# Kernel tuning notes

Measured on AMD Instinct MI355X. Metric: run time of the kernel, lower is better.

The kernel has to match this reference:

```python
import jax, jax.numpy as jnp
import numpy as np

WINDOW = 7
SHIFT = 3
HEADS = 4


def _rel_pos_index(w):
    # same construction as ShiftedWindowAttention.__init__ (numpy, static)
    coords = np.stack(np.meshgrid(np.arange(w), np.arange(w), indexing='ij'))  # [2,w,w]
    cf = coords.reshape(2, -1)                       # [2, w*w]
    rc = (cf[:, :, None] - cf[:, None, :]).transpose(1, 2, 0)  # [L,L,2]
    rc[:, :, 0] += w - 1
    rc[:, :, 1] += w - 1
    rc[:, :, 0] *= 2 * w - 1
    return rc.sum(-1).reshape(-1)                    # [L*L]


def _attn_mask(H, W, w, s):
    # cyclic-shift attention mask, static numpy constant
    m = np.zeros((H, W))
    slices = ((0, -w), (-w, -s), (-s, None))
    cnt = 0
    for hs in slices:
        for ws in slices:
            m[hs[0]:hs[1], ws[0]:ws[1]] = cnt
            cnt += 1
    m = m.reshape(H // w, w, W // w, w).transpose(0, 2, 1, 3).reshape(-1, w * w)  # [nwin, L]
    d = m[:, None, :] - m[:, :, None]                # [nwin, L, L]
    return np.where(d != 0, -100.0, 0.0).astype(np.float32)


def setup_inputs() -> dict:
    key = jax.random.key(0)
    ks = jax.random.split(key, 6)
    B, H, W, C = 64, 56, 56, 128
    return {
        'x': jax.random.normal(ks[0], (B, H, W, C), dtype=jnp.float32),
        'qkv_weight': jax.random.normal(ks[1], (3 * C, C), dtype=jnp.float32) * 0.02,
        'qkv_bias': jax.random.normal(ks[2], (3 * C,), dtype=jnp.float32) * 0.02,
        'proj_weight': jax.random.normal(ks[3], (C, C), dtype=jnp.float32) * 0.02,
        'proj_bias': jax.random.normal(ks[4], (C,), dtype=jnp.float32) * 0.02,
        'rel_bias_table': jax.random.normal(ks[5], ((2 * WINDOW - 1) ** 2, HEADS), dtype=jnp.float32) * 0.02,
    }


def reference(x, qkv_weight, qkv_bias, proj_weight, proj_bias, rel_bias_table):
    B, H, W, C = x.shape
    w, s, h = WINDOW, SHIFT, HEADS
    d = C // h
    nH, nW = H // w, W // w
    nwin = nH * nW
    L = w * w

    # relative position bias: [h, L, L]
    bias = rel_bias_table[jnp.asarray(_rel_pos_index(w))].reshape(L, L, h).transpose(2, 0, 1)

    # cyclic shift + window partition -> [B*nwin, L, C]
    xs = jnp.roll(x, (-s, -s), axis=(1, 2))
    xw = xs.reshape(B, nH, w, nW, w, C).transpose(0, 1, 3, 2, 4, 5).reshape(B * nwin, L, C)

    # fused qkv projection (F.linear: x @ W.T + b)
    qkv = (xw @ qkv_weight.T + qkv_bias).reshape(B * nwin, L, 3, h, d).transpose(2, 0, 3, 1, 4)
    q, k, v = qkv[0] * (d ** -0.5), qkv[1], qkv[2]   # each [B*nwin, h, L, d]

    attn = jnp.einsum('nhqd,nhkd->nhqk', q, k) + bias[None]
    mask = jnp.asarray(_attn_mask(H, W, w, s))       # [nwin, L, L]
    attn = attn.reshape(B, nwin, h, L, L) + mask[None, :, None]
    attn = jax.nn.softmax(attn.reshape(B * nwin, h, L, L), axis=-1)

    out = jnp.einsum('nhqk,nhkd->nhqd', attn, v).transpose(0, 2, 1, 3).reshape(B * nwin, L, C)
    out = out @ proj_weight.T + proj_bias

    # window merge + reverse shift -> [B, H, W, C]
    out = out.reshape(B, nH, nW, w, w, C).transpose(0, 1, 3, 2, 4, 5).reshape(B, H, W, C)
    return jnp.roll(out, (s, s), axis=(1, 2))
```

## Files before the change

kernel.cpp:

```cpp
#include <hip/hip_runtime.h>

typedef __attribute__((ext_vector_type(8))) short short8;
typedef __attribute__((ext_vector_type(4))) float f32x4;

static __device__ __forceinline__ unsigned short f2bf(float f) {
  union { float f; unsigned int u; } v; v.f = f;
  unsigned int r = v.u + 0x7FFFu + ((v.u >> 16) & 1u);
  return (unsigned short)(r >> 16);
}
static __device__ __forceinline__ unsigned int pack2(float a, float b) {
  return (unsigned int)f2bf(a) | ((unsigned int)f2bf(b) << 16);
}

#define KO 0
#define VO 2560
#define PO 4864
#define WSTRIDE 7424

__global__ __launch_bounds__(256) void k_prep(const float* __restrict__ wq,
    const float* __restrict__ wp, const float* __restrict__ tbl,
    unsigned short* __restrict__ dq, unsigned short* __restrict__ dp,
    unsigned short* __restrict__ biasH) {
  const int n = blockIdx.x * 256 + threadIdx.x;
  if (n < 384 * 128) dq[n] = f2bf(wq[n]);
  if (n < 128 * 128) dp[n] = f2bf(wp[n]);
  if (n < 65536) {
    const int j = n & 63, i = (n >> 6) & 63;
    const int h = (n >> 12) & 3, bb = (n >> 14) & 1, aa = (n >> 15) & 1;
    float val;
    if (i >= 49) val = 0.0f;
    else if (j >= 49) val = -1e30f;
    else {
      const int ih = i / 7, iw = i - ih * 7, jh = j / 7, jw = j - jh * 7;
      const int didx = (ih - jh + 6) * 13 + (iw - jw + 6);
      const int irg = (aa ? (ih < 4 ? 3 : 6) : 0) + (bb ? (iw < 4 ? 1 : 2) : 0);
      const int jrg = (aa ? (jh < 4 ? 3 : 6) : 0) + (bb ? (jw < 4 ? 1 : 2) : 0);
      val = tbl[didx * 4 + h] - (irg != jrg ? 100.0f : 0.0f);
    }
    biasH[n] = f2bf(val);
  }
}

__global__ __launch_bounds__(256) void k_prepx(const float* __restrict__ x,
    unsigned short* __restrict__ xw) {
  const int idx = blockIdx.x * 256 + threadIdx.x;
  const int row = idx >> 4;
  const int c8 = idx & 15;
  const int win = row / 49;
  const int t = row - win * 49;
  const int b = win >> 6, wl = win & 63;
  const int wh = wl >> 3, ww = wl & 7;
  const int th = t / 7, tw = t - th * 7;
  int sh = wh * 7 + th + 3; if (sh >= 56) sh -= 56;
  int sw = ww * 7 + tw + 3; if (sw >= 56) sw -= 56;
  const float4* src = (const float4*)(x + (((size_t)(b * 56 + sh)) * 56 + sw) * 128 + c8 * 8);
  float4 fa = src[0], fb = src[1];
  uint4 u;
  u.x = pack2(fa.x, fa.y); u.y = pack2(fa.z, fa.w);
  u.z = pack2(fb.x, fb.y); u.w = pack2(fb.z, fb.w);
  *(uint4*)(xw + (size_t)row * 128 + c8 * 8) = u;
}

__global__ __launch_bounds__(256, 2) void k_fused(const unsigned short* __restrict__ xw,
    const unsigned short* __restrict__ Wq, const float* __restrict__ qb,
    const unsigned short* __restrict__ Wp, const float* __restrict__ pb,
    const unsigned short* __restrict__ biasH, float* __restrict__ out) {
  __shared__ __align__(16) unsigned short lds[4 * WSTRIDE];
  const int tid = threadIdx.x;
  const int win = blockIdx.x;
  const int b = win >> 6, wl = win & 63;
  const int wh = wl >> 3, ww = wl & 7;
  const int wv = tid >> 6, ln = tid & 63;
  const int l15 = ln & 15, l4 = ln >> 4;
  unsigned short* W = lds + wv * WSTRIDE;

  const unsigned short* bmB = biasH
      + ((((wh == 7 ? 2 : 0) + (ww == 7 ? 1 : 0)) * 4 + wv) << 12)
      + l15 * 64 + 4 * l4;
  uint2 bm16[4][4];
#pragma unroll
  for (int mt = 0; mt < 4; ++mt)
#pragma unroll
    for (int nt = 0; nt < 4; ++nt)
      bm16[mt][nt] = *(const uint2*)(bmB + mt * 1024 + nt * 16);

  const unsigned short* rp[4];
  bool vld[4];
#pragma unroll
  for (int mt = 0; mt < 4; ++mt) {
    const int t = mt * 16 + l15;
    vld[mt] = (t < 49);
    rp[mt] = xw + ((size_t)win * 49 + (vld[mt] ? t : 0)) * 128;
  }
  int nrow[6];
#pragma unroll
  for (int j = 0; j < 6; ++j)
    nrow[j] = (j >> 1) * 128 + wv * 32 + (j & 1) * 16 + l15;

  const f32x4 z4 = {0.f, 0.f, 0.f, 0.f};
  f32x4 aS[4][4], aV[4][2];
#pragma unroll
  for (int mt = 0; mt < 4; ++mt) {
#pragma unroll
    for (int j = 0; j < 4; ++j) aS[mt][j] = z4;
#pragma unroll
    for (int j = 0; j < 2; ++j) aV[mt][j] = z4;
  }
#pragma unroll
  for (int ks = 0; ks < 4; ++ks) {
    short8 af[4], bf[6];
#pragma unroll
    for (int mt = 0; mt < 4; ++mt) {
      uint4 u = *(const uint4*)(rp[mt] + ks * 32 + l4 * 8);
      u.x = vld[mt] ? u.x : 0u; u.y = vld[mt] ? u.y : 0u;
      u.z = vld[mt] ? u.z : 0u; u.w = vld[mt] ? u.w : 0u;
      af[mt] = *(short8*)&u;
    }
#pragma unroll
    for (int j = 0; j < 6; ++j)
      bf[j] = *(const short8*)&Wq[(size_t)nrow[j] * 128 + ks * 32 + l4 * 8];
#pragma unroll
    for (int mt = 0; mt < 4; ++mt) {
#pragma unroll
      for (int j = 0; j < 4; ++j)
        aS[mt][j] = __builtin_amdgcn_mfma_f32_16x16x32_bf16(bf[j], af[mt], aS[mt][j], 0, 0, 0);
#pragma unroll
      for (int j = 0; j < 2; ++j)
        aV[mt][j] = __builtin_amdgcn_mfma_f32_16x16x32_bf16(af[mt], bf[4 + j], aV[mt][j], 0, 0, 0);
    }
  }
  {
    const float SC = 0.17677669529663687f;
    const float4 bq0 = *(const float4*)(qb + wv * 32 + 4 * l4);
    const float4 bq1 = *(const float4*)(qb + wv * 32 + 16 + 4 * l4);
    const float4 bk0 = *(const float4*)(qb + 128 + wv * 32 + 4 * l4);
    const float4 bk1 = *(const float4*)(qb + 128 + wv * 32 + 16 + 4 * l4);
    const float bv0 = qb[256 + wv * 32 + l15];
    const float bv1 = qb[256 + wv * 32 + 16 + l15];
#pragma unroll
    for (int mt = 0; mt < 4; ++mt) {
      const int t = mt * 16 + l15;
      uint2 u;
      u.x = pack2((aS[mt][0][0] + bq0.x) * SC, (aS[mt][0][1] + bq0.y) * SC);
      u.y = pack2((aS[mt][0][2] + bq0.z) * SC, (aS[mt][0][3] + bq0.w) * SC);
      *(uint2*)&W[PO + t * 40 + 4 * l4] = u;
      u.x = pack2((aS[mt][1][0] + bq1.x) * SC, (aS[mt][1][1] + bq1.y) * SC);
      u.y = pack2((aS[mt][1][2] + bq1.z) * SC, (aS[mt][1][3] + bq1.w) * SC);
      *(uint2*)&W[PO + t * 40 + 16 + 4 * l4] = u;
      u.x = pack2(aS[mt][2][0] + bk0.x, aS[mt][2][1] + bk0.y);
      u.y = pack2(aS[mt][2][2] + bk0.z, aS[mt][2][3] + bk0.w);
      *(uint2*)&W[KO + t * 40 + 4 * l4] = u;
      u.x = pack2(aS[mt][3][0] + bk1.x, aS[mt][3][1] + bk1.y);
      u.y = pack2(aS[mt][3][2] + bk1.z, aS[mt][3][3] + bk1.w);
      *(uint2*)&W[KO + t * 40 + 16 + 4 * l4] = u;
      u.x = pack2(aV[mt][0][0] + bv0, aV[mt][0][1] + bv0);
      u.y = pack2(aV[mt][0][2] + bv0, aV[mt][0][3] + bv0);
      *(uint2*)&W[VO + l15 * 72 + mt * 16 + 4 * l4] = u;
      u.x = pack2(aV[mt][1][0] + bv1, aV[mt][1][1] + bv1);
      u.y = pack2(aV[mt][1][2] + bv1, aV[mt][1][3] + bv1);
      *(uint2*)&W[VO + (16 + l15) * 72 + mt * 16 + 4 * l4] = u;
    }
  }

  f32x4 s[4][4];
#pragma unroll
  for (int mt = 0; mt < 4; ++mt)
#pragma unroll
    for (int nt = 0; nt < 4; ++nt) s[mt][nt] = z4;
  {
    short8 qf[4], kf[4];
#pragma unroll
    for (int mt = 0; mt < 4; ++mt)
      qf[mt] = *(const short8*)&W[PO + (mt * 16 + l15) * 40 + l4 * 8];
#pragma unroll
    for (int nt = 0; nt < 4; ++nt)
      kf[nt] = *(const short8*)&W[KO + (nt * 16 + l15) * 40 + l4 * 8];
#pragma unroll
    for (int mt = 0; mt < 4; ++mt)
#pragma unroll
      for (int nt = 0; nt < 4; ++nt)
        s[mt][nt] = __builtin_amdgcn_mfma_f32_16x16x32_bf16(kf[nt], qf[mt], s[mt][nt], 0, 0, 0);
  }

  float pmax[4] = {-1e30f, -1e30f, -1e30f, -1e30f};
#pragma unroll
  for (int mt = 0; mt < 4; ++mt) {
#pragma unroll
    for (int nt = 0; nt < 4; ++nt) {
      const uint2 u = bm16[mt][nt];
      s[mt][nt][0] += __uint_as_float(u.x << 16);
      s[mt][nt][1] += __uint_as_float(u.x & 0xFFFF0000u);
      s[mt][nt][2] += __uint_as_float(u.y << 16);
      s[mt][nt][3] += __uint_as_float(u.y & 0xFFFF0000u);
      pmax[mt] = fmaxf(pmax[mt], fmaxf(fmaxf(s[mt][nt][0], s[mt][nt][1]),
                                       fmaxf(s[mt][nt][2], s[mt][nt][3])));
    }
  }
  float inv[4];
#pragma unroll
  for (int mt = 0; mt < 4; ++mt) {
    float m0 = pmax[mt];
    m0 = fmaxf(m0, __shfl_xor(m0, 16));
    m0 = fmaxf(m0, __shfl_xor(m0, 32));
    float sum = 0.0f;
#pragma unroll
    for (int nt = 0; nt < 4; ++nt)
#pragma unroll
      for (int r = 0; r < 4; ++r) {
        const float v = s[mt][nt][r];
        const float e = (v > -1e29f) ? __expf(v - m0) : 0.0f;
        s[mt][nt][r] = e;
        sum += e;
      }
    sum += __shfl_xor(sum, 16);
    sum += __shfl_xor(sum, 32);
    inv[mt] = 1.0f / sum;
  }

  f32x4 o[4][2];
#pragma unroll
  for (int mt = 0; mt < 4; ++mt)
#pragma unroll
    for (int dt = 0; dt < 2; ++dt) o[mt][dt] = z4;
#pragma unroll
  for (int mt = 0; mt < 4; ++mt) {
    const int i = mt * 16 + l15;
    if (i < 49) {
#pragma unroll
      for (int nt = 0; nt < 2; ++nt) {
        uint2 u;
        u.x = pack2(s[mt][nt][0] * inv[mt], s[mt][nt][1] * inv[mt]);
        u.y = pack2(s[mt][nt][2] * inv[mt], s[mt][nt][3] * inv[mt]);
        *(uint2*)&W[PO + i * 40 + nt * 16 + 4 * l4] = u;
      }
    }
  }
  {
    short8 pa[4], vb[2];
#pragma unroll
    for (int mt = 0; mt < 4; ++mt)
      pa[mt] = *(const short8*)&W[PO + (mt * 16 + l15) * 40 + l4 * 8];
#pragma unroll
    for (int dt = 0; dt < 2; ++dt)
      vb[dt] = *(const short8*)&W[VO + (dt * 16 + l15) * 72 + l4 * 8];
#pragma unroll
    for (int mt = 0; mt < 4; ++mt)
#pragma unroll
      for (int dt = 0; dt < 2; ++dt)
        o[mt][dt] = __builtin_amdgcn_mfma_f32_16x16x32_bf16(vb[dt], pa[mt], o[mt][dt], 0, 0, 0);
  }
#pragma unroll
  for (int mt = 0; mt < 4; ++mt) {
    const int i = mt * 16 + l15;
    if (i < 49) {
#pragma unroll
      for (int nt = 2; nt < 4; ++nt) {
        uint2 u;
        u.x = pack2(s[mt][nt][0] * inv[mt], s[mt][nt][1] * inv[mt]);
        u.y = pack2(s[mt][nt][2] * inv[mt], s[mt][nt][3] * inv[mt]);
        *(uint2*)&W[PO + i * 40 + (nt - 2) * 16 + 4 * l4] = u;
      }
    }
  }
  {
    short8 pa[4], vb[2];
#pragma unroll
    for (int mt = 0; mt < 4; ++mt)
      pa[mt] = *(const short8*)&W[PO + (mt * 16 + l15) * 40 + l4 * 8];
#pragma unroll
    for (int dt = 0; dt < 2; ++dt)
      vb[dt] = *(const short8*)&W[VO + (dt * 16 + l15) * 72 + 32 + l4 * 8];
#pragma unroll
    for (int mt = 0; mt < 4; ++mt)
#pragma unroll
      for (int dt = 0; dt < 2; ++dt)
        o[mt][dt] = __builtin_amdgcn_mfma_f32_16x16x32_bf16(vb[dt], pa[mt], o[mt][dt], 0, 0, 0);
  }
#pragma unroll
  for (int mt = 0; mt < 4; ++mt) {
    const int t = mt * 16 + l15;
#pragma unroll
    for (int dt = 0; dt < 2; ++dt) {
      uint2 u;
      u.x = pack2(o[mt][dt][0], o[mt][dt][1]);
      u.y = pack2(o[mt][dt][2], o[mt][dt][3]);
      *(uint2*)&W[KO + t * 40 + dt * 16 + 4 * l4] = u;
    }
  }
  __syncthreads();

  const float4 pbv0 = *(const float4*)(pb + wv * 32 + 4 * l4);
  const float4 pbv1 = *(const float4*)(pb + wv * 32 + 16 + 4 * l4);
  f32x4 c2[4][2];
#pragma unroll
  for (int mt = 0; mt < 4; ++mt)
#pragma unroll
    for (int nt = 0; nt < 2; ++nt) c2[mt][nt] = z4;
#pragma unroll
  for (int ks = 0; ks < 4; ++ks) {
    short8 a2[4], bp[2];
#pragma unroll
    for (int mt = 0; mt < 4; ++mt)
      a2[mt] = *(const short8*)&lds[ks * WSTRIDE + KO + (mt * 16 + l15) * 40 + l4 * 8];
#pragma unroll
    for (int nt = 0; nt < 2; ++nt)
      bp[nt] = *(const short8*)&Wp[(size_t)(wv * 32 + nt * 16 + l15) * 128 + ks * 32 + l4 * 8];
#pragma unroll
    for (int mt = 0; mt < 4; ++mt)
#pragma unroll
      for (int nt = 0; nt < 2; ++nt)
        c2[mt][nt] = __builtin_amdgcn_mfma_f32_16x16x32_bf16(bp[nt], a2[mt], c2[mt][nt], 0, 0, 0);
  }
#pragma unroll
  for (int mt = 0; mt < 4; ++mt) {
    const int t = mt * 16 + l15;
    if (t < 49) {
      const int th = t / 7, tw = t - th * 7;
      int y = wh * 7 + th + 3; if (y >= 56) y -= 56;
      int xx = ww * 7 + tw + 3; if (xx >= 56) xx -= 56;
      float* dstp = out + (((size_t)(b * 56 + y)) * 56 + xx) * 128 + wv * 32 + 4 * l4;
      float4 v0, v1;
      v0.x = c2[mt][0][0] + pbv0.x; v0.y = c2[mt][0][1] + pbv0.y;
      v0.z = c2[mt][0][2] + pbv0.z; v0.w = c2[mt][0][3] + pbv0.w;
      *(float4*)(dstp) = v0;
      v1.x = c2[mt][1][0] + pbv1.x; v1.y = c2[mt][1][1] + pbv1.y;
      v1.z = c2[mt][1][2] + pbv1.z; v1.w = c2[mt][1][3] + pbv1.w;
      *(float4*)(dstp + 16) = v1;
    }
  }
}

extern "C" void kernel_launch(void* const* d_in, const int* in_sizes, int n_in,
                              void* d_out, int out_size, void* d_ws, size_t ws_size,
                              hipStream_t stream) {
  const float* x     = (const float*)d_in[0];
  const float* qkvw  = (const float*)d_in[1];
  const float* qkvb  = (const float*)d_in[2];
  const float* projw = (const float*)d_in[3];
  const float* projb = (const float*)d_in[4];
  const float* table = (const float*)d_in[5];
  float* out = (float*)d_out;
  char* ws = (char*)d_ws;
  unsigned short* xw    = (unsigned short*)ws;
  unsigned short* Wq    = (unsigned short*)(ws + 51380224);
  unsigned short* Wp    = (unsigned short*)(ws + 51478528);
  unsigned short* biasH = (unsigned short*)(ws + 51511296);

  k_prep<<<dim3(256), dim3(256), 0, stream>>>(qkvw, projw, table, Wq, Wp, biasH);
  k_prepx<<<dim3(12544), dim3(256), 0, stream>>>(x, xw);
  k_fused<<<dim3(4096), dim3(256), 0, stream>>>(xw, Wq, qkvb, Wp, projb, biasH, out);
}
```

Measured before the change: 167.5 us.

## Split each window's query rows across two blocks to raise parallelism and cut registers

Each window is now handled by two blocks, and each block computes half of the query rows, 32 of the 64 padded tokens. K and V are still computed in full by both blocks. The V projection is moved into its own second pass, and the shared-memory layout is shrunk, to lower register pressure and LDS use, and the min-blocks launch bound is dropped. The intent is higher occupancy and more blocks in flight. The cost is that the K/V projections are computed twice per window, and the xw/Wq reads are repeated.

Measured after the change: 560.2 us. +234.4%, slower.

```diff
diff --git a/kernel.cpp b/kernel.cpp
--- a/kernel.cpp
+++ b/kernel.cpp
@@ -12,10 +12,10 @@
   return (unsigned int)f2bf(a) | ((unsigned int)f2bf(b) << 16);
 }
 
-#define KO 0
-#define VO 2560
-#define PO 4864
-#define WSTRIDE 7424
+#define QP 0
+#define KB 1280
+#define VB 3840
+#define WSTR 6144
 
 __global__ __launch_bounds__(256) void k_prep(const float* __restrict__ wq,
     const float* __restrict__ wp, const float* __restrict__ tbl,
@@ -61,25 +61,26 @@
   *(uint4*)(xw + (size_t)row * 128 + c8 * 8) = u;
 }
 
-__global__ __launch_bounds__(256, 2) void k_fused(const unsigned short* __restrict__ xw,
+__global__ __launch_bounds__(256) void k_fused(const unsigned short* __restrict__ xw,
     const unsigned short* __restrict__ Wq, const float* __restrict__ qb,
     const unsigned short* __restrict__ Wp, const float* __restrict__ pb,
     const unsigned short* __restrict__ biasH, float* __restrict__ out) {
-  __shared__ __align__(16) unsigned short lds[4 * WSTRIDE];
+  __shared__ __align__(16) unsigned short lds[4 * WSTR];
   const int tid = threadIdx.x;
-  const int win = blockIdx.x;
+  const int bid = blockIdx.x;
+  const int win = bid >> 1, half = bid & 1;
   const int b = win >> 6, wl = win & 63;
   const int wh = wl >> 3, ww = wl & 7;
   const int wv = tid >> 6, ln = tid & 63;
   const int l15 = ln & 15, l4 = ln >> 4;
-  unsigned short* W = lds + wv * WSTRIDE;
+  unsigned short* W = lds + wv * WSTR;
 
   const unsigned short* bmB = biasH
       + ((((wh == 7 ? 2 : 0) + (ww == 7 ? 1 : 0)) * 4 + wv) << 12)
-      + l15 * 64 + 4 * l4;
-  uint2 bm16[4][4];
-#pragma unroll
-  for (int mt = 0; mt < 4; ++mt)
+      + half * 2048 + l15 * 64 + 4 * l4;
+  uint2 bm16[2][4];
+#pragma unroll
+  for (int mt = 0; mt < 2; ++mt)
 #pragma unroll
     for (int nt = 0; nt < 4; ++nt)
       bm16[mt][nt] = *(const uint2*)(bmB + mt * 1024 + nt * 16);
@@ -92,23 +93,20 @@
     vld[mt] = (t < 49);
     rp[mt] = xw + ((size_t)win * 49 + (vld[mt] ? t : 0)) * 128;
   }
-  int nrow[6];
-#pragma unroll
-  for (int j = 0; j < 6; ++j)
-    nrow[j] = (j >> 1) * 128 + wv * 32 + (j & 1) * 16 + l15;
-
   const f32x4 z4 = {0.f, 0.f, 0.f, 0.f};
-  f32x4 aS[4][4], aV[4][2];
-#pragma unroll
-  for (int mt = 0; mt < 4; ++mt) {
-#pragma unroll
-    for (int j = 0; j < 4; ++j) aS[mt][j] = z4;
-#pragma unroll
-    for (int j = 0; j < 2; ++j) aV[mt][j] = z4;
-  }
+
+  f32x4 aQ[2][2], aK[4][2];
+#pragma unroll
+  for (int mt = 0; mt < 2; ++mt)
+#pragma unroll
+    for (int dt = 0; dt < 2; ++dt) aQ[mt][dt] = z4;
+#pragma unroll
+  for (int nt = 0; nt < 4; ++nt)
+#pragma unroll
+    for (int dt = 0; dt < 2; ++dt) aK[nt][dt] = z4;
 #pragma unroll
   for (int ks = 0; ks < 4; ++ks) {
-    short8 af[4], bf[6];
+    short8 af[4], bfq[2], bfk[2];
 #pragma unroll
     for (int mt = 0; mt < 4; ++mt) {
       uint4 u = *(const uint4*)(rp[mt] + ks * 32 + l4 * 8);
@@ -117,17 +115,20 @@
       af[mt] = *(short8*)&u;
     }
 #pragma unroll
-    for (int j = 0; j < 6; ++j)
-      bf[j] = *(const short8*)&Wq[(size_t)nrow[j] * 128 + ks * 32 + l4 * 8];
-#pragma unroll
-    for (int mt = 0; mt < 4; ++mt) {
-#pragma unroll
-      for (int j = 0; j < 4; ++j)
-        aS[mt][j] = __builtin_amdgcn_mfma_f32_16x16x32_bf16(bf[j], af[mt], aS[mt][j], 0, 0, 0);
-#pragma unroll
-      for (int j = 0; j < 2; ++j)
-        aV[mt][j] = __builtin_amdgcn_mfma_f32_16x16x32_bf16(af[mt], bf[4 + j], aV[mt][j], 0, 0, 0);
-    }
+    for (int dt = 0; dt < 2; ++dt) {
+      bfq[dt] = *(const short8*)&Wq[(size_t)(wv * 32 + dt * 16 + l15) * 128 + ks * 32 + l4 * 8];
+      bfk[dt] = *(const short8*)&Wq[(size_t)(128 + wv * 32 + dt * 16 + l15) * 128 + ks * 32 + l4 * 8];
+    }
+#pragma unroll
+    for (int mt = 0; mt < 2; ++mt)
+#pragma unroll
+      for (int dt = 0; dt < 2; ++dt)
+        aQ[mt][dt] = __builtin_amdgcn_mfma_f32_16x16x32_bf16(bfq[dt], af[half * 2 + mt], aQ[mt][dt], 0, 0, 0);
+#pragma unroll
+    for (int nt = 0; nt < 4; ++nt)
+#pragma unroll
+      for (int dt = 0; dt < 2; ++dt)
+        aK[nt][dt] = __builtin_amdgcn_mfma_f32_16x16x32_bf16(bfk[dt], af[nt], aK[nt][dt], 0, 0, 0);
   }
   {
     const float SC = 0.17677669529663687f;
@@ -135,56 +136,92 @@
     const float4 bq1 = *(const float4*)(qb + wv * 32 + 16 + 4 * l4);
     const float4 bk0 = *(const float4*)(qb + 128 + wv * 32 + 4 * l4);
     const float4 bk1 = *(const float4*)(qb + 128 + wv * 32 + 16 + 4 * l4);
+#pragma unroll
+    for (int mt = 0; mt < 2; ++mt) {
+      const int tl = mt * 16 + l15;
+      uint2 u;
+      u.x = pack2((aQ[mt][0][0] + bq0.x) * SC, (aQ[mt][0][1] + bq0.y) * SC);
+      u.y = pack2((aQ[mt][0][2] + bq0.z) * SC, (aQ[mt][0][3] + bq0.w) * SC);
+      *(uint2*)&W[QP + tl * 40 + 4 * l4] = u;
+      u.x = pack2((aQ[mt][1][0] + bq1.x) * SC, (aQ[mt][1][1] + bq1.y) * SC);
+      u.y = pack2((aQ[mt][1][2] + bq1.z) * SC, (aQ[mt][1][3] + bq1.w) * SC);
+      *(uint2*)&W[QP + tl * 40 + 16 + 4 * l4] = u;
+    }
+#pragma unroll
+    for (int nt = 0; nt < 4; ++nt) {
+      const int tg = nt * 16 + l15;
+      uint2 u;
+      u.x = pack2(aK[nt][0][0] + bk0.x, aK[nt][0][1] + bk0.y);
+      u.y = pack2(aK[nt][0][2] + bk0.z, aK[nt][0][3] + bk0.w);
+      *(uint2*)&W[KB + tg * 40 + 4 * l4] = u;
+      u.x = pack2(aK[nt][1][0] + bk1.x, aK[nt][1][1] + bk1.y);
+      u.y = pack2(aK[nt][1][2] + bk1.z, aK[nt][1][3] + bk1.w);
+      *(uint2*)&W[KB + tg * 40 + 16 + 4 * l4] = u;
+    }
+  }
+
+  f32x4 aV[4][2];
+#pragma unroll
+  for (int nt = 0; nt < 4; ++nt)
+#pragma unroll
+    for (int dt = 0; dt < 2; ++dt) aV[nt][dt] = z4;
+#pragma unroll
+  for (int ks = 0; ks < 4; ++ks) {
+    short8 af[4], bfv[2];
+#pragma unroll
+    for (int mt = 0; mt < 4; ++mt) {
+      uint4 u = *(const uint4*)(rp[mt] + ks * 32 + l4 * 8);
+      u.x = vld[mt] ? u.x : 0u; u.y = vld[mt] ? u.y : 0u;
+      u.z = vld[mt] ? u.z : 0u; u.w = vld[mt] ? u.w : 0u;
+      af[mt] = *(short8*)&u;
+    }
+#pragma unroll
+    for (int dt = 0; dt < 2; ++dt)
+      bfv[dt] = *(const short8*)&Wq[(size_t)(256 + wv * 32 + dt * 16 + l15) * 128 + ks * 32 + l4 * 8];
+#pragma unroll
+    for (int nt = 0; nt < 4; ++nt)
+#pragma unroll
+      for (int dt = 0; dt < 2; ++dt)
+        aV[nt][dt] = __builtin_amdgcn_mfma_f32_16x16x32_bf16(af[nt], bfv[dt], aV[nt][dt], 0, 0, 0);
+  }
+  {
     const float bv0 = qb[256 + wv * 32 + l15];
     const float bv1 = qb[256 + wv * 32 + 16 + l15];
 #pragma unroll
-    for (int mt = 0; mt < 4; ++mt) {
-      const int t = mt * 16 + l15;
+    for (int nt = 0; nt < 4; ++nt) {
       uint2 u;
-      u.x = pack2((aS[mt][0][0] + bq0.x) * SC, (aS[mt][0][1] + bq0.y) * SC);
-      u.y = pack2((aS[mt][0][2] + bq0.z) * SC, (aS[mt][0][3] + bq0.w) * SC);
-      *(uint2*)&W[PO + t * 40 + 4 * l4] = u;
-      u.x = pack2((aS[mt][1][0] + bq1.x) * SC, (aS[mt][1][1] + bq1.y) * SC);
-      u.y = pack2((aS[mt][1][2] + bq1.z) * SC, (aS[mt][1][3] + bq1.w) * SC);
-      *(uint2*)&W[PO + t * 40 + 16 + 4 * l4] = u;
-      u.x = pack2(aS[mt][2][0] + bk0.x, aS[mt][2][1] + bk0.y);
-      u.y = pack2(aS[mt][2][2] + bk0.z, aS[mt][2][3] + bk0.w);
-      *(uint2*)&W[KO + t * 40 + 4 * l4] = u;
-      u.x = pack2(aS[mt][3][0] + bk1.x, aS[mt][3][1] + bk1.y);
-      u.y = pack2(aS[mt][3][2] + bk1.z, aS[mt][3][3] + bk1.w);
-      *(uint2*)&W[KO + t * 40 + 16 + 4 * l4] = u;
-      u.x = pack2(aV[mt][0][0] + bv0, aV[mt][0][1] + bv0);
-      u.y = pack2(aV[mt][0][2] + bv0, aV[mt][0][3] + bv0);
-      *(uint2*)&W[VO + l15 * 72 + mt * 16 + 4 * l4] = u;
-      u.x = pack2(aV[mt][1][0] + bv1, aV[mt][1][1] + bv1);
-      u.y = pack2(aV[mt][1][2] + bv1, aV[mt][1][3] + bv1);
-      *(uint2*)&W[VO + (16 + l15) * 72 + mt * 16 + 4 * l4] = u;
-    }
-  }
-
-  f32x4 s[4][4];
-#pragma unroll
-  for (int mt = 0; mt < 4; ++mt)
+      u.x = pack2(aV[nt][0][0] + bv0, aV[nt][0][1] + bv0);
+      u.y = pack2(aV[nt][0][2] + bv0, aV[nt][0][3] + bv0);
+      *(uint2*)&W[VB + l15 * 72 + nt * 16 + 4 * l4] = u;
+      u.x = pack2(aV[nt][1][0] + bv1, aV[nt][1][1] + bv1);
+      u.y = pack2(aV[nt][1][2] + bv1, aV[nt][1][3] + bv1);
+      *(uint2*)&W[VB + (16 + l15) * 72 + nt * 16 + 4 * l4] = u;
+    }
+  }
+
+  f32x4 s[2][4];
+#pragma unroll
+  for (int mt = 0; mt < 2; ++mt)
 #pragma unroll
     for (int nt = 0; nt < 4; ++nt) s[mt][nt] = z4;
   {
-    short8 qf[4], kf[4];
-#pragma unroll
-    for (int mt = 0; mt < 4; ++mt)
-      qf[mt] = *(const short8*)&W[PO + (mt * 16 + l15) * 40 + l4 * 8];
-#pragma unroll
-    for (int nt = 0; nt < 4; ++nt)
-      kf[nt] = *(const short8*)&W[KO + (nt * 16 + l15) * 40 + l4 * 8];
-#pragma unroll
-    for (int mt = 0; mt < 4; ++mt)
+    short8 qf[2], kf[4];
+#pragma unroll
+    for (int mt = 0; mt < 2; ++mt)
+      qf[mt] = *(const short8*)&W[QP + (mt * 16 + l15) * 40 + l4 * 8];
+#pragma unroll
+    for (int nt = 0; nt < 4; ++nt)
+      kf[nt] = *(const short8*)&W[KB + (nt * 16 + l15) * 40 + l4 * 8];
+#pragma unroll
+    for (int mt = 0; mt < 2; ++mt)
 #pragma unroll
       for (int nt = 0; nt < 4; ++nt)
         s[mt][nt] = __builtin_amdgcn_mfma_f32_16x16x32_bf16(kf[nt], qf[mt], s[mt][nt], 0, 0, 0);
   }
 
-  float pmax[4] = {-1e30f, -1e30f, -1e30f, -1e30f};
-#pragma unroll
-  for (int mt = 0; mt < 4; ++mt) {
+  float pmax[2] = {-1e30f, -1e30f};
+#pragma unroll
+  for (int mt = 0; mt < 2; ++mt) {
 #pragma unroll
     for (int nt = 0; nt < 4; ++nt) {
       const uint2 u = bm16[mt][nt];
@@ -196,9 +233,9 @@
                                        fmaxf(s[mt][nt][2], s[mt][nt][3])));
     }
   }
-  float inv[4];
-#pragma unroll
-  for (int mt = 0; mt < 4; ++mt) {
+  float inv[2];
+#pragma unroll
+  for (int mt = 0; mt < 2; ++mt) {
     float m0 = pmax[mt];
     m0 = fmaxf(m0, __shfl_xor(m0, 16));
     m0 = fmaxf(m0, __shfl_xor(m0, 32));
@@ -217,105 +254,80 @@
     inv[mt] = 1.0f / sum;
   }
 
-  f32x4 o[4][2];
-#pragma unroll
-  for (int mt = 0; mt < 4; ++mt)
+  f32x4 o[2][2];
+#pragma unroll
+  for (int mt = 0; mt < 2; ++mt)
 #pragma unroll
     for (int dt = 0; dt < 2; ++dt) o[mt][dt] = z4;
 #pragma unroll
-  for (int mt = 0; mt < 4; ++mt) {
-    const int i = mt * 16 + l15;
-    if (i < 49) {
-#pragma unroll
-      for (int nt = 0; nt < 2; ++nt) {
-        uint2 u;
-        u.x = pack2(s[mt][nt][0] * inv[mt], s[mt][nt][1] * inv[mt]);
-        u.y = pack2(s[mt][nt][2] * inv[mt], s[mt][nt][3] * inv[mt]);
-        *(uint2*)&W[PO + i * 40 + nt * 16 + 4 * l4] = u;
+  for (int pass = 0; pass < 2; ++pass) {
+#pragma unroll
+    for (int mt = 0; mt < 2; ++mt) {
+      const int ig = half * 32 + mt * 16 + l15;
+      if (ig < 49) {
+#pragma unroll
+        for (int nt = 0; nt < 2; ++nt) {
+          const int ntp = pass * 2 + nt;
+          uint2 u;
+          u.x = pack2(s[mt][ntp][0] * inv[mt], s[mt][ntp][1] * inv[mt]);
+          u.y = pack2(s[mt][ntp][2] * inv[mt], s[mt][ntp][3] * inv[mt]);
+          *(uint2*)&W[QP + (mt * 16 + l15) * 40 + nt * 16 + 4 * l4] = u;
+        }
       }
     }
-  }
-  {
-    short8 pa[4], vb[2];
-#pragma unroll
-    for (int mt = 0; mt < 4; ++mt)
-      pa[mt] = *(const short8*)&W[PO + (mt * 16 + l15) * 40 + l4 * 8];
+    short8 pa[2], vb[2];
+#pragma unroll
+    for (int mt = 0; mt < 2; ++mt)
+      pa[mt] = *(const short8*)&W[QP + (mt * 16 + l15) * 40 + l4 * 8];
 #pragma unroll
     for (int dt = 0; dt < 2; ++dt)
-      vb[dt] = *(const short8*)&W[VO + (dt * 16 + l15) * 72 + l4 * 8];
-#pragma unroll
-    for (int mt = 0; mt < 4; ++mt)
+      vb[dt] = *(const short8*)&W[VB + (dt * 16 + l15) * 72 + pass * 32 + l4 * 8];
+#pragma unroll
+    for (int mt = 0; mt < 2; ++mt)
 #pragma unroll
       for (int dt = 0; dt < 2; ++dt)
         o[mt][dt] = __builtin_amdgcn_mfma_f32_16x16x32_bf16(vb[dt], pa[mt], o[mt][dt], 0, 0, 0);
   }
 #pragma unroll
-  for (int mt = 0; mt < 4; ++mt) {
-    const int i = mt * 16 + l15;
-    if (i < 49) {
-#pragma unroll
-      for (int nt = 2; nt < 4; ++nt) {
-        uint2 u;
-        u.x = pack2(s[mt][nt][0] * inv[mt], s[mt][nt][1] * inv[mt]);
-        u.y = pack2(s[mt][nt][2] * inv[mt], s[mt][nt][3] * inv[mt]);
-        *(uint2*)&W[PO + i * 40 + (nt - 2) * 16 + 4 * l4] = u;
-      }
-    }
-  }
-  {
-    short8 pa[4], vb[2];
-#pragma unroll
-    for (int mt = 0; mt < 4; ++mt)
-      pa[mt] = *(const short8*)&W[PO + (mt * 16 + l15) * 40 + l4 * 8];
-#pragma unroll
-    for (int dt = 0; dt < 2; ++dt)
-      vb[dt] = *(const short8*)&W[VO + (dt * 16 + l15) * 72 + 32 + l4 * 8];
-#pragma unroll
-    for (int mt = 0; mt < 4; ++mt)
-#pragma unroll
-      for (int dt = 0; dt < 2; ++dt)
-        o[mt][dt] = __builtin_amdgcn_mfma_f32_16x16x32_bf16(vb[dt], pa[mt], o[mt][dt], 0, 0, 0);
-  }
-#pragma unroll
-  for (int mt = 0; mt < 4; ++mt) {
-    const int t = mt * 16 + l15;
+  for (int mt = 0; mt < 2; ++mt) {
+    const int tl = mt * 16 + l15;
 #pragma unroll
     for (int dt = 0; dt < 2; ++dt) {
       uint2 u;
       u.x = pack2(o[mt][dt][0], o[mt][dt][1]);
       u.y = pack2(o[mt][dt][2], o[mt][dt][3]);
-      *(uint2*)&W[KO + t * 40 + dt * 16 + 4 * l4] = u;
+      *(uint2*)&W[QP + tl * 40 + dt * 16 + 4 * l4] = u;
     }
   }
   __syncthreads();
 
   const float4 pbv0 = *(const float4*)(pb + wv * 32 + 4 * l4);
   const float4 pbv1 = *(const float4*)(pb + wv * 32 + 16 + 4 * l4);
-  f32x4 c2[4][2];
-#pragma unroll
-  for (int mt = 0; mt < 4; ++mt)
+  f32x4 c2[2][2];
+#pragma unroll
+  for (int mt = 0; mt < 2; ++mt)
 #pragma unroll
     for (int nt = 0; nt < 2; ++nt) c2[mt][nt] = z4;
 #pragma unroll
   for (int ks = 0; ks < 4; ++ks) {
-    short8 a2[4], bp[2];
-#pragma unroll
-    for (int mt = 0; mt < 4; ++mt)
-      a2[mt] = *(const short8*)&lds[ks * WSTRIDE + KO + (mt * 16 + l15) * 40 + l4 * 8];
+    short8 a2[2], bp[2];
+#pragma unroll
+    for (int mt = 0; mt < 2; ++mt)
+      a2[mt] = *(const short8*)&lds[ks * WSTR + QP + (mt * 16 + l15) * 40 + l4 * 8];
 #pragma unroll
     for (int nt = 0; nt < 2; ++nt)
       bp[nt] = *(const short8*)&Wp[(size_t)(wv * 32 + nt * 16 + l15) * 128 + ks * 32 + l4 * 8];
 #pragma unroll
-    for (int mt = 0; mt < 4; ++mt)
+    for (int mt = 0; mt < 2; ++mt)
 #pragma unroll
       for (int nt = 0; nt < 2; ++nt)
         c2[mt][nt] = __builtin_amdgcn_mfma_f32_16x16x32_bf16(bp[nt], a2[mt], c2[mt][nt], 0, 0, 0);
   }
 #pragma unroll
-  for (int mt = 0; mt < 4; ++mt) {
-    const int t = mt * 16 + l15;
-    if (t < 49) {
-      const int th = t / 7, tw = t - th * 7;
+  for (int mt = 0; mt < 2; ++mt) {
+    const int tg = half * 32 + mt * 16 + l15;
+    if (tg < 49) {
+      const int th = tg / 7, tw = tg - th * 7;
       int y = wh * 7 + th + 3; if (y >= 56) y -= 56;
       int xx = ww * 7 + tw + 3; if (xx >= 56) xx -= 56;
       float* dstp = out + (((size_t)(b * 56 + y)) * 56 + xx) * 128 + wv * 32 + 4 * l4;
@@ -348,5 +360,5 @@
 
   k_prep<<<dim3(256), dim3(256), 0, stream>>>(qkvw, projw, table, Wq, Wp, biasH);
   k_prepx<<<dim3(12544), dim3(256), 0, stream>>>(x, xw);
-  k_fused<<<dim3(4096), dim3(256), 0, stream>>>(xw, Wq, qkvb, Wp, projb, biasH, out);
-}
+  k_fused<<<dim3(8192), dim3(256), 0, stream>>>(xw, Wq, qkvb, Wp, projb, biasH, out);
+}
```
